# Kernel tuning notes

Hardware: AMD Instinct MI355X
Metric: run time of the kernel (lower is better)

The kernel has to match this reference:

```python
import jax, jax.numpy as jnp
import numpy as np
from jax import lax

B, N, D, H, K = 4096, 25, 256, 8, 3  # batch*frames, nodes, d_model, heads, conv kernel


def _layernorm(x, g, b, eps=1e-5):
    mu = jnp.mean(x, axis=-1, keepdims=True)
    var = jnp.var(x, axis=-1, keepdims=True)
    return (x - mu) * lax.rsqrt(var + eps) * g + b


def _conv1d(x_bdn, w):
    # x_bdn: [B, D, N], w: [D_out, D_in, K], padding=K//2 (same as torch Conv1d)
    return lax.conv_general_dilated(x_bdn, w, window_strides=(1,),
                                    padding=[(K // 2, K // 2)],
                                    dimension_numbers=('NCH', 'OIH', 'NCH'))


def setup_inputs() -> dict:
    key = jax.random.key(0)
    ks = jax.random.split(key, 12)
    x = jax.random.normal(ks[0], (B, N, D), dtype=jnp.float32)
    # symmetric adjacency with self-loops (skeleton graph surrogate)
    a = jax.random.bernoulli(ks[1], 0.3, (N, N))
    adj = a | a.T | jnp.eye(N, dtype=bool)
    cs = 1.0 / np.sqrt(D * K)
    wq = jax.random.normal(ks[2], (D, D, K), dtype=jnp.float32) * cs
    wk = jax.random.normal(ks[3], (D, D, K), dtype=jnp.float32) * cs
    wv = jax.random.normal(ks[4], (D, D, K), dtype=jnp.float32) * cs
    gq = jnp.ones((D,), jnp.float32); bq = jnp.zeros((D,), jnp.float32)
    gk = jnp.ones((D,), jnp.float32); bk = jnp.zeros((D,), jnp.float32)
    gv = jnp.ones((D,), jnp.float32); bv = jnp.zeros((D,), jnp.float32)
    rel_table = jax.random.normal(ks[5], (2 * N - 1, H), dtype=jnp.float32) * 0.02
    local_bias = jnp.zeros((H, N, N), jnp.float32)
    wo = jax.random.normal(ks[6], (D, D), dtype=jnp.float32) * (1.0 / np.sqrt(D))
    bo = jnp.zeros((D,), jnp.float32)
    return dict(x=x, adj=adj, wq=wq, wk=wk, wv=wv, gq=gq, bq=bq, gk=gk, bk=bk,
                gv=gv, bv=bv, rel_table=rel_table, local_bias=local_bias, wo=wo, bo=bo)


def reference(x, adj, wq, wk, wv, gq, bq, gk, bk, gv, bv, rel_table, local_bias, wo, bo):
    b, n, d = x.shape
    h = local_bias.shape[0]
    dk = d // h
    xp = x.transpose(0, 2, 1)  # [B, D, N]
    # conv QKV projection over node axis + per-projection LayerNorm + residual
    q = x + _layernorm(_conv1d(xp, wq).transpose(0, 2, 1), gq, bq)
    k = x + _layernorm(_conv1d(xp, wk).transpose(0, 2, 1), gk, bk)
    v = x + _layernorm(_conv1d(xp, wv).transpose(0, 2, 1), gv, bv)
    qh = q.reshape(b, n, h, dk).transpose(0, 2, 1, 3)  # [B, H, N, dk]
    kh = k.reshape(b, n, h, dk).transpose(0, 2, 1, 3)
    vh = v.reshape(b, n, h, dk).transpose(0, 2, 1, 3)
    scores = jnp.einsum('bhnd,bhmd->bhnm', qh, kh) / np.sqrt(dk)
    # relative positional bias over node indices
    coords = jnp.arange(n)
    idx = coords[:, None] - coords[None, :] + n - 1  # [N, N]
    rel = rel_table[idx].transpose(2, 0, 1)  # [H, N, N]
    scores = scores + rel[None] + local_bias[None]
    # adjacency mask (local attention): non-neighbors -> -inf
    scores = jnp.where(adj[None, None], scores, jnp.finfo(scores.dtype).min)
    attn = jax.nn.softmax(scores, axis=-1)
    out = jnp.einsum('bhnm,bhmd->bhnd', attn, vh)  # [B, H, N, dk]
    out = out.transpose(0, 2, 1, 3).reshape(b, n, d)
    return out @ wo.T + bo
```

## Files before the change

### kernel.cpp

```cpp
#include <hip/hip_runtime.h>

#define BB 4096
#define NN 25
#define DD 256
#define HH 8
#define DKH 32
#define MM (BB*NN)

typedef __bf16 bf16;
typedef bf16 bf16x8 __attribute__((ext_vector_type(8)));
typedef bf16 bf16x4 __attribute__((ext_vector_type(4)));
typedef float f32x4 __attribute__((ext_vector_type(4)));
typedef _Float16 h16;
typedef h16 h16x2 __attribute__((ext_vector_type(2)));
typedef h16 h16x4 __attribute__((ext_vector_type(4)));
typedef h16 h16x8 __attribute__((ext_vector_type(8)));

__device__ __forceinline__ void async_load16(const void* g, void* l) {
  __builtin_amdgcn_global_load_lds(
      (const __attribute__((address_space(1))) unsigned int*)g,
      (__attribute__((address_space(3))) unsigned int*)l, 16, 0, 0);
}

__global__ __launch_bounds__(256) void k_prep_xpad(const float* __restrict__ x,
                                                   bf16* __restrict__ xpad) {
  int idx = (blockIdx.x * 256 + threadIdx.x) * 8;
  const int total = BB * 27 * 256;
  if (idx >= total) return;
  int b = idx / (27 * 256);
  int rem = idx - b * 27 * 256;
  int j = rem >> 8;
  int d = rem & 255;
  bf16x8 o;
  if (j >= 1 && j <= 25) {
    const float* src = x + ((b * 25 + (j - 1)) * 256 + d);
    #pragma unroll
    for (int t = 0; t < 8; ++t) o[t] = (bf16)src[t];
  } else {
    #pragma unroll
    for (int t = 0; t < 8; ++t) o[t] = (bf16)0.0f;
  }
  *(bf16x8*)(xpad + idx) = o;
}

__global__ __launch_bounds__(256) void k_prep_misc(
    const float* __restrict__ wq, const float* __restrict__ wk, const float* __restrict__ wv,
    const float* __restrict__ rel, const float* __restrict__ lb, const float* __restrict__ wo,
    const void* __restrict__ adj_raw,
    bf16* __restrict__ Wt, bf16* __restrict__ woB, float* __restrict__ mb) {
  const int NWT = 768 * 768;
  const int NWO = 256 * 256;
  const int NMB = HH * NN * 32;
  const int total = NWT + NWO + NMB;
  for (int i = blockIdx.x * blockDim.x + threadIdx.x; i < total; i += gridDim.x * blockDim.x) {
    if (i < NWT) {
      int j = i / 768, kk = i - j * 768;
      int proj = j >> 8, jo = j & 255;
      int tap = kk >> 8, di = kk & 255;
      const float* w = (proj == 0) ? wq : ((proj == 1) ? wk : wv);
      Wt[i] = (bf16)w[(jo * 256 + di) * 3 + tap];
    } else if (i < NWT + NWO) {
      int t = i - NWT;
      woB[t] = (bf16)wo[t];
    } else {
      int t = i - NWT - NWO;
      int pair = t >> 5;
      int m = t & 31;
      int h = pair / 25, ii = pair - h * 25;
      float v = -1e30f;
      if (m < 25) {
        const unsigned char* bytes = (const unsigned char*)adj_raw;
        bool u8 = false;
        for (int s = 0; s < 625; ++s) {
          if ((s & 3) && bytes[s]) { u8 = true; break; }
        }
        int amask = u8 ? (bytes[ii * 25 + m] ? 1 : 0)
                       : (((const int*)adj_raw)[ii * 25 + m] ? 1 : 0);
        if (amask)
          v = rel[(ii - m + 24) * HH + h] + lb[h * 625 + ii * 25 + m];
      }
      mb[t] = v;
    }
  }
}

__global__ __launch_bounds__(256) void k_qkv_gemm(const bf16* __restrict__ xpad,
                                                  const bf16* __restrict__ Wt,
                                                  bf16* __restrict__ conv) {
  __shared__ bf16 As[128 * 32];
  __shared__ bf16 Bs[128 * 32];
  const int L = blockIdx.x;
  const int X = L & 7;
  const int t = L >> 3;
  const int n0 = (t % 6) * 128;
  const int m0 = (X + 8 * (t / 6)) * 128;
  const int tid = threadIdx.x;
  const int wave = tid >> 6, lane = tid & 63;
  const int quad = lane >> 4, t16 = lane & 15;
  const int wr = wave >> 1, wc = wave & 1;

  f32x4 acc[4][4];
  #pragma unroll
  for (int i = 0; i < 4; ++i)
    #pragma unroll
    for (int j = 0; j < 4; ++j) acc[i][j] = (f32x4){0.f, 0.f, 0.f, 0.f};

  const bf16* baseA[2];
  const bf16* baseB[2];
  #pragma unroll
  for (int r = 0; r < 2; ++r) {
    int c = r * 256 + wave * 64 + lane;
    int row = c >> 2, sub = c & 3;
    int gm = m0 + row;
    int b = gm / 25;
    int n = gm - b * 25;
    baseA[r] = xpad + (b * 27 + n) * 256 + sub * 8;
    baseB[r] = Wt + (n0 + row) * 768 + sub * 8;
  }

  for (int ks = 0; ks < 768; ks += 32) {
    const int tap = ks >> 8;
    const int d0 = ks & 255;
    #pragma unroll
    for (int r = 0; r < 2; ++r)
      async_load16(baseA[r] + tap * 256 + d0, As + (r * 256 + wave * 64) * 8);
    #pragma unroll
    for (int r = 0; r < 2; ++r)
      async_load16(baseB[r] + ks, Bs + (r * 256 + wave * 64) * 8);
    asm volatile("s_waitcnt vmcnt(0)" ::: "memory");
    __syncthreads();

    bf16x8 af[4], bfr[4];
    #pragma unroll
    for (int i = 0; i < 4; ++i)
      af[i] = *(const bf16x8*)(As + (wr * 64 + i * 16 + t16) * 32 + quad * 8);
    #pragma unroll
    for (int j = 0; j < 4; ++j)
      bfr[j] = *(const bf16x8*)(Bs + (wc * 64 + j * 16 + t16) * 32 + quad * 8);
    #pragma unroll
    for (int i = 0; i < 4; ++i)
      #pragma unroll
      for (int j = 0; j < 4; ++j)
        acc[i][j] = __builtin_amdgcn_mfma_f32_16x16x32_bf16(af[i], bfr[j], acc[i][j], 0, 0, 0);
    __syncthreads();
  }

  #pragma unroll
  for (int i = 0; i < 4; ++i)
    #pragma unroll
    for (int j = 0; j < 4; ++j) {
      int col = n0 + wc * 64 + j * 16 + t16;
      #pragma unroll
      for (int r = 0; r < 4; ++r) {
        int rowm = m0 + wr * 64 + i * 16 + quad * 4 + r;
        conv[rowm * 768 + col] = (bf16)acc[i][j][r];
      }
    }
}

__global__ __launch_bounds__(256, 4) void k_attn3(
    const bf16* __restrict__ conv, const float* __restrict__ x,
    const float* __restrict__ gq, const float* __restrict__ bq,
    const float* __restrict__ gk, const float* __restrict__ bk,
    const float* __restrict__ gv, const float* __restrict__ bv,
    const float* __restrict__ mb, bf16* __restrict__ attnout) {
  __shared__ bf16 Cs[19456];
  const int b = blockIdx.x;
  const int tid = threadIdx.x;
  const int wave = tid >> 6, lane = tid & 63;

  const char* slab = (const char*)(conv + (size_t)b * 19200);
  for (int c = wave; c < 38; c += 4)
    async_load16(slab + c * 1024 + lane * 16, (char*)Cs + c * 1024);
  asm volatile("s_waitcnt vmcnt(0)" ::: "memory");
  __syncthreads();

  for (int rowi = wave; rowi < 75; rowi += 4) {
    int n = rowi / 3;
    int p = rowi - n * 3;
    const int off = n * 768 + p * 256 + lane * 4;
    bf16x4 cv = *(const bf16x4*)(Cs + off);
    float v0 = (float)cv[0], v1 = (float)cv[1], v2 = (float)cv[2], v3 = (float)cv[3];
    float s = v0 + v1 + v2 + v3;
    float ss = v0 * v0 + v1 * v1 + v2 * v2 + v3 * v3;
    #pragma unroll
    for (int o = 32; o; o >>= 1) {
      s += __shfl_xor(s, o);
      ss += __shfl_xor(ss, o);
    }
    float mu = s * (1.0f / 256.0f);
    float var = ss * (1.0f / 256.0f) - mu * mu;
    float rs = rsqrtf(var + 1e-5f);
    const float* gsel = (p == 0) ? gq : ((p == 1) ? gk : gv);
    const float* bsel = (p == 0) ? bq : ((p == 1) ? bk : bv);
    const int dbase = lane * 4;
    f32x4 gg = *(const f32x4*)(gsel + dbase);
    f32x4 b2 = *(const f32x4*)(bsel + dbase);
    f32x4 xv = *(const f32x4*)(x + ((size_t)(b * 25 + n)) * 256 + dbase);
    h16x4 o;
    o[0] = (h16)((v0 - mu) * rs * gg[0] + b2[0] + xv[0]);
    o[1] = (h16)((v1 - mu) * rs * gg[1] + b2[1] + xv[1]);
    o[2] = (h16)((v2 - mu) * rs * gg[2] + b2[2] + xv[2]);
    o[3] = (h16)((v3 - mu) * rs * gg[3] + b2[3] + xv[3]);
    *(h16x4*)((h16*)Cs + off) = o;
  }
  __syncthreads();

  const h16* Ch = (const h16*)Cs;
  if (tid < HH * NN) {
    const int h = tid / 25;
    const int i = tid - h * 25;

    h16x2 qv[16];
    const h16x2* qp = (const h16x2*)(Ch + i * 768 + h * 32);
    #pragma unroll
    for (int c = 0; c < 16; ++c) qv[c] = qp[c];

    float mrow[28];
    const float* mbp = mb + (h * 25 + i) * 32;
    #pragma unroll
    for (int c = 0; c < 7; ++c) *(f32x4*)(mrow + c * 4) = *(const f32x4*)(mbp + c * 4);

    const float scale = 0.17677669529663687f;
    float sc[25];
    #pragma unroll
    for (int m = 0; m < 25; ++m) {
      const h16x2* kr = (const h16x2*)(Ch + m * 768 + 256 + h * 32);
      float d = 0.f;
      #pragma unroll
      for (int c = 0; c < 16; ++c)
        d = __builtin_amdgcn_fdot2(qv[c], kr[c], d, false);
      sc[m] = d * scale + mrow[m];
    }

    float mx = sc[0];
    #pragma unroll
    for (int m = 1; m < 25; ++m) mx = fmaxf(mx, sc[m]);
    float sum = 0.f;
    #pragma unroll
    for (int m = 0; m < 25; ++m) { sc[m] = __expf(sc[m] - mx); sum += sc[m]; }
    const float inv = 1.0f / sum;

    h16x2 acc[16];
    #pragma unroll
    for (int j = 0; j < 16; ++j) acc[j] = (h16x2){(h16)0.f, (h16)0.f};
    #pragma unroll
    for (int m = 0; m < 25; ++m) {
      h16 w = (h16)(sc[m] * inv);
      h16x2 wp = {w, w};
      const h16x2* vr = (const h16x2*)(Ch + m * 768 + 512 + h * 32);
      #pragma unroll
      for (int j = 0; j < 16; ++j)
        acc[j] = wp * vr[j] + acc[j];
    }

    bf16* dst = attnout + ((size_t)b * 25 + i) * 256 + h * 32;
    #pragma unroll
    for (int c = 0; c < 4; ++c) {
      bf16x8 o;
      #pragma unroll
      for (int j = 0; j < 4; ++j) {
        o[2 * j]     = (bf16)(float)acc[c * 4 + j][0];
        o[2 * j + 1] = (bf16)(float)acc[c * 4 + j][1];
      }
      *(bf16x8*)(dst + c * 8) = o;
    }
  }
}

__global__ __launch_bounds__(256) void k_outproj(const bf16* __restrict__ attn,
                                                 const bf16* __restrict__ woB,
                                                 const float* __restrict__ bo,
                                                 float* __restrict__ out) {
  __shared__ bf16 As[128 * 32];
  __shared__ bf16 Bs[128 * 32];
  const int L = blockIdx.x;
  const int X = L & 7;
  const int t = L >> 3;
  const int n0 = (t & 1) * 128;
  const int m0 = (X + 8 * (t >> 1)) * 128;
  const int tid = threadIdx.x;
  const int wave = tid >> 6, lane = tid & 63;
  const int quad = lane >> 4, t16 = lane & 15;
  const int wr = wave >> 1, wc = wave & 1;

  f32x4 acc[4][4];
  #pragma unroll
  for (int i = 0; i < 4; ++i)
    #pragma unroll
    for (int j = 0; j < 4; ++j) acc[i][j] = (f32x4){0.f, 0.f, 0.f, 0.f};

  const bf16* baseA[2];
  const bf16* baseB[2];
  #pragma unroll
  for (int r = 0; r < 2; ++r) {
    int c = r * 256 + wave * 64 + lane;
    int row = c >> 2, sub = c & 3;
    baseA[r] = attn + (m0 + row) * 256 + sub * 8;
    baseB[r] = woB + (n0 + row) * 256 + sub * 8;
  }

  for (int ks = 0; ks < 256; ks += 32) {
    #pragma unroll
    for (int r = 0; r < 2; ++r)
      async_load16(baseA[r] + ks, As + (r * 256 + wave * 64) * 8);
    #pragma unroll
    for (int r = 0; r < 2; ++r)
      async_load16(baseB[r] + ks, Bs + (r * 256 + wave * 64) * 8);
    asm volatile("s_waitcnt vmcnt(0)" ::: "memory");
    __syncthreads();

    bf16x8 af[4], bfr[4];
    #pragma unroll
    for (int i = 0; i < 4; ++i)
      af[i] = *(const bf16x8*)(As + (wr * 64 + i * 16 + t16) * 32 + quad * 8);
    #pragma unroll
    for (int j = 0; j < 4; ++j)
      bfr[j] = *(const bf16x8*)(Bs + (wc * 64 + j * 16 + t16) * 32 + quad * 8);
    #pragma unroll
    for (int i = 0; i < 4; ++i)
      #pragma unroll
      for (int j = 0; j < 4; ++j)
        acc[i][j] = __builtin_amdgcn_mfma_f32_16x16x32_bf16(af[i], bfr[j], acc[i][j], 0, 0, 0);
    __syncthreads();
  }

  #pragma unroll
  for (int j = 0; j < 4; ++j) {
    int col = n0 + wc * 64 + j * 16 + t16;
    float bb = bo[col];
    #pragma unroll
    for (int i = 0; i < 4; ++i)
      #pragma unroll
      for (int r = 0; r < 4; ++r) {
        int rowm = m0 + wr * 64 + i * 16 + quad * 4 + r;
        out[rowm * 256 + col] = acc[i][j][r] + bb;
      }
  }
}

extern "C" void kernel_launch(void* const* d_in, const int* in_sizes, int n_in,
                              void* d_out, int out_size, void* d_ws, size_t ws_size,
                              hipStream_t stream) {
  (void)in_sizes; (void)n_in; (void)out_size; (void)ws_size;
  const float* x  = (const float*)d_in[0];
  const void*  adj = d_in[1];
  const float* wq = (const float*)d_in[2];
  const float* wk = (const float*)d_in[3];
  const float* wv = (const float*)d_in[4];
  const float* gq = (const float*)d_in[5];
  const float* bq = (const float*)d_in[6];
  const float* gk = (const float*)d_in[7];
  const float* bk = (const float*)d_in[8];
  const float* gv = (const float*)d_in[9];
  const float* bv = (const float*)d_in[10];
  const float* rel = (const float*)d_in[11];
  const float* lb = (const float*)d_in[12];
  const float* wo = (const float*)d_in[13];
  const float* bo = (const float*)d_in[14];
  float* out = (float*)d_out;

  char* ws = (char*)d_ws;
  size_t off = 0;
  auto alloc = [&](size_t bytes) -> void* {
    void* p = ws + off;
    off += (bytes + 255) & ~(size_t)255;
    return p;
  };
  bf16* xpad = (bf16*)alloc((size_t)BB * 27 * 256 * 2);
  bf16* conv = (bf16*)alloc((size_t)MM * 768 * 2);
  bf16* attn = (bf16*)alloc((size_t)MM * 256 * 2);
  bf16* Wt   = (bf16*)alloc((size_t)768 * 768 * 2);
  bf16* woB  = (bf16*)alloc((size_t)256 * 256 * 2);
  float* mb  = (float*)alloc((size_t)HH * NN * 32 * 4);

  hipLaunchKernelGGL(k_prep_xpad, dim3(13824), dim3(256), 0, stream, x, xpad);
  hipLaunchKernelGGL(k_prep_misc, dim3(512), dim3(256), 0, stream,
                     wq, wk, wv, rel, lb, wo, adj, Wt, woB, mb);
  hipLaunchKernelGGL(k_qkv_gemm, dim3(4800), dim3(256), 0, stream, xpad, Wt, conv);
  hipLaunchKernelGGL(k_attn3, dim3(4096), dim3(256), 0, stream,
                     conv, x, gq, bq, gk, bk, gv, bv, mb, attn);
  hipLaunchKernelGGL(k_outproj, dim3(1600), dim3(256), 0, stream, attn, woB, bo, out);
}
```

Measured before the change: 556.5 us.

## Rewrite QKV conv GEMM as 256x256 double-buffered 8-wave pipelined kernel

Replaces the 128x128, 4-wave, single-buffered QKV GEMM with a 256x256 tile, 8-wave, 64-wide K-step kernel. It double-buffers LDS with async global-to-LDS loads, uses XOR-swizzled LDS layouts, and interleaves MFMA phases with the next loads under scheduling barriers and s_setprio. Block indices are remapped so consecutive blocks share tiles. The aim is to hide global load latency behind compute and raise data reuse per block. The cost is 128KB of LDS per block, heavier register use, and many barriers per K-step.

Result: no change. 549.4 us (-1.3%).

```diff
diff --git a/kernel.cpp b/kernel.cpp
--- a/kernel.cpp
+++ b/kernel.cpp
@@ -21,6 +21,10 @@
       (const __attribute__((address_space(1))) unsigned int*)g,
       (__attribute__((address_space(3))) unsigned int*)l, 16, 0, 0);
 }
+
+#define SCHED_FENCE() __builtin_amdgcn_sched_barrier(0)
+#define BARRIER() do { SCHED_FENCE(); __builtin_amdgcn_s_barrier(); SCHED_FENCE(); } while (0)
+#define WAIT_LGKM0() do { asm volatile("s_waitcnt lgkmcnt(0)" ::: "memory"); SCHED_FENCE(); } while (0)
 
 __global__ __launch_bounds__(256) void k_prep_xpad(const float* __restrict__ x,
                                                    bf16* __restrict__ xpad) {
@@ -84,76 +88,176 @@
   }
 }
 
-__global__ __launch_bounds__(256) void k_qkv_gemm(const bf16* __restrict__ xpad,
-                                                  const bf16* __restrict__ Wt,
-                                                  bf16* __restrict__ conv) {
-  __shared__ bf16 As[128 * 32];
-  __shared__ bf16 Bs[128 * 32];
+__global__ __launch_bounds__(512, 2) void k_qkv_gemm8(const bf16* __restrict__ xpad,
+                                                      const bf16* __restrict__ Wt,
+                                                      bf16* __restrict__ conv) {
+  __shared__ bf16 Ab[2][256 * 64];
+  __shared__ bf16 Bb[2][256 * 64];
+
   const int L = blockIdx.x;
-  const int X = L & 7;
-  const int t = L >> 3;
-  const int n0 = (t % 6) * 128;
-  const int m0 = (X + 8 * (t / 6)) * 128;
+  const int sw = (L & 7) * 150 + (L >> 3);
+  const int n0 = (sw % 3) * 256;
+  const int m0 = (sw / 3) * 256;
+
   const int tid = threadIdx.x;
-  const int wave = tid >> 6, lane = tid & 63;
-  const int quad = lane >> 4, t16 = lane & 15;
-  const int wr = wave >> 1, wc = wave & 1;
-
-  f32x4 acc[4][4];
-  #pragma unroll
-  for (int i = 0; i < 4; ++i)
-    #pragma unroll
-    for (int j = 0; j < 4; ++j) acc[i][j] = (f32x4){0.f, 0.f, 0.f, 0.f};
-
-  const bf16* baseA[2];
-  const bf16* baseB[2];
-  #pragma unroll
-  for (int r = 0; r < 2; ++r) {
-    int c = r * 256 + wave * 64 + lane;
-    int row = c >> 2, sub = c & 3;
+  const int lane = tid & 63, wave = tid >> 6;
+  const int t16 = lane & 15, quad = lane >> 4;
+  const int wr = wave >> 2, wc = wave & 3;
+
+  const int srow = tid >> 3;
+  const int sc = ((tid & 7) << 4) ^ ((srow & 7) << 4);
+  int aOff[4], bOff[4];
+  #pragma unroll
+  for (int q = 0; q < 4; ++q) {
+    int row = q * 64 + srow;
     int gm = m0 + row;
     int b = gm / 25;
     int n = gm - b * 25;
-    baseA[r] = xpad + (b * 27 + n) * 256 + sub * 8;
-    baseB[r] = Wt + (n0 + row) * 768 + sub * 8;
-  }
-
-  for (int ks = 0; ks < 768; ks += 32) {
-    const int tap = ks >> 8;
-    const int d0 = ks & 255;
-    #pragma unroll
-    for (int r = 0; r < 2; ++r)
-      async_load16(baseA[r] + tap * 256 + d0, As + (r * 256 + wave * 64) * 8);
-    #pragma unroll
-    for (int r = 0; r < 2; ++r)
-      async_load16(baseB[r] + ks, Bs + (r * 256 + wave * 64) * 8);
-    asm volatile("s_waitcnt vmcnt(0)" ::: "memory");
-    __syncthreads();
-
-    bf16x8 af[4], bfr[4];
-    #pragma unroll
-    for (int i = 0; i < 4; ++i)
-      af[i] = *(const bf16x8*)(As + (wr * 64 + i * 16 + t16) * 32 + quad * 8);
-    #pragma unroll
-    for (int j = 0; j < 4; ++j)
-      bfr[j] = *(const bf16x8*)(Bs + (wc * 64 + j * 16 + t16) * 32 + quad * 8);
-    #pragma unroll
-    for (int i = 0; i < 4; ++i)
-      #pragma unroll
-      for (int j = 0; j < 4; ++j)
-        acc[i][j] = __builtin_amdgcn_mfma_f32_16x16x32_bf16(af[i], bfr[j], acc[i][j], 0, 0, 0);
-    __syncthreads();
-  }
-
-  #pragma unroll
-  for (int i = 0; i < 4; ++i)
+    aOff[q] = (b * 27 + n) * 512 + sc;
+    bOff[q] = (n0 + row) * 1536 + sc;
+  }
+
+  const int axr = (t16 & 7) << 3;
+  int aoffs[2], boffs[2];
+  #pragma unroll
+  for (int kk = 0; kk < 2; ++kk) {
+    aoffs[kk] = (wr * 128 + t16) * 64 + ((kk * 32 + quad * 8) ^ axr);
+    boffs[kk] = (wc * 64 + t16) * 64 + ((kk * 32 + quad * 8) ^ axr);
+  }
+
+  f32x4 acc[8][4];
+  #pragma unroll
+  for (int i = 0; i < 8; ++i)
+    #pragma unroll
+    for (int j = 0; j < 4; ++j) acc[i][j] = (f32x4){0.f, 0.f, 0.f, 0.f};
+
+  #pragma unroll
+  for (int tt = 0; tt < 2; ++tt) {
+    char* lb = (char*)&Bb[tt][0] + wave * 1024;
+    char* la = (char*)&Ab[tt][0] + wave * 1024;
+    #pragma unroll
+    for (int q = 0; q < 4; ++q)
+      async_load16((const char*)Wt + bOff[q] + tt * 128, lb + q * 8192);
+    #pragma unroll
+    for (int q = 0; q < 4; ++q)
+      async_load16((const char*)xpad + aOff[q] + tt * 128, la + q * 8192);
+  }
+  asm volatile("s_waitcnt vmcnt(8)" ::: "memory");
+  SCHED_FENCE();
+  BARRIER();
+
+  for (int u = 0; u < 12; ++u) {
+    const int buf = u & 1;
+    const bf16* Ac = &Ab[buf][0];
+    const bf16* Bc = &Bb[buf][0];
+    const int st = u + 2;
+
+    bf16x8 aF[8], bF[8];
+
+    #pragma unroll
+    for (int i = 0; i < 4; ++i)
+      #pragma unroll
+      for (int kk = 0; kk < 2; ++kk)
+        aF[i * 2 + kk] = *(const bf16x8*)(Ac + aoffs[kk] + i * 1024);
+    #pragma unroll
+    for (int j = 0; j < 2; ++j)
+      #pragma unroll
+      for (int kk = 0; kk < 2; ++kk)
+        bF[j * 2 + kk] = *(const bf16x8*)(Bc + boffs[kk] + j * 1024);
+    BARRIER();
+    WAIT_LGKM0();
+    __builtin_amdgcn_s_setprio(1);
+    #pragma unroll
+    for (int i = 0; i < 4; ++i)
+      #pragma unroll
+      for (int j = 0; j < 2; ++j)
+        #pragma unroll
+        for (int kk = 0; kk < 2; ++kk)
+          acc[i][j] = __builtin_amdgcn_mfma_f32_16x16x32_bf16(
+              aF[i * 2 + kk], bF[j * 2 + kk], acc[i][j], 0, 0, 0);
+    __builtin_amdgcn_s_setprio(0);
+    BARRIER();
+
+    #pragma unroll
+    for (int j = 0; j < 2; ++j)
+      #pragma unroll
+      for (int kk = 0; kk < 2; ++kk)
+        bF[4 + j * 2 + kk] = *(const bf16x8*)(Bc + boffs[kk] + (2 + j) * 1024);
+    BARRIER();
+    WAIT_LGKM0();
+    __builtin_amdgcn_s_setprio(1);
+    #pragma unroll
+    for (int i = 0; i < 4; ++i)
+      #pragma unroll
+      for (int j = 0; j < 2; ++j)
+        #pragma unroll
+        for (int kk = 0; kk < 2; ++kk)
+          acc[i][2 + j] = __builtin_amdgcn_mfma_f32_16x16x32_bf16(
+              aF[i * 2 + kk], bF[4 + j * 2 + kk], acc[i][2 + j], 0, 0, 0);
+    __builtin_amdgcn_s_setprio(0);
+    BARRIER();
+
+    #pragma unroll
+    for (int i = 0; i < 4; ++i)
+      #pragma unroll
+      for (int kk = 0; kk < 2; ++kk)
+        aF[i * 2 + kk] = *(const bf16x8*)(Ac + aoffs[kk] + (4 + i) * 1024);
+    if (st < 12) {
+      char* lb = (char*)&Bb[buf][0] + wave * 1024;
+      #pragma unroll
+      for (int q = 0; q < 4; ++q)
+        async_load16((const char*)Wt + bOff[q] + st * 128, lb + q * 8192);
+    }
+    BARRIER();
+    WAIT_LGKM0();
+    __builtin_amdgcn_s_setprio(1);
+    #pragma unroll
+    for (int i = 0; i < 4; ++i)
+      #pragma unroll
+      for (int j = 0; j < 2; ++j)
+        #pragma unroll
+        for (int kk = 0; kk < 2; ++kk)
+          acc[4 + i][j] = __builtin_amdgcn_mfma_f32_16x16x32_bf16(
+              aF[i * 2 + kk], bF[j * 2 + kk], acc[4 + i][j], 0, 0, 0);
+    __builtin_amdgcn_s_setprio(0);
+    BARRIER();
+
+    if (st < 12) {
+      char* la = (char*)&Ab[buf][0] + wave * 1024;
+      const int ka = (st >> 2) * 512 + (st & 3) * 128;
+      #pragma unroll
+      for (int q = 0; q < 4; ++q)
+        async_load16((const char*)xpad + aOff[q] + ka, la + q * 8192);
+    }
+    BARRIER();
+    __builtin_amdgcn_s_setprio(1);
+    #pragma unroll
+    for (int i = 0; i < 4; ++i)
+      #pragma unroll
+      for (int j = 0; j < 2; ++j)
+        #pragma unroll
+        for (int kk = 0; kk < 2; ++kk)
+          acc[4 + i][2 + j] = __builtin_amdgcn_mfma_f32_16x16x32_bf16(
+              aF[i * 2 + kk], bF[4 + j * 2 + kk], acc[4 + i][2 + j], 0, 0, 0);
+    __builtin_amdgcn_s_setprio(0);
+    if (u < 10) {
+      asm volatile("s_waitcnt vmcnt(8)" ::: "memory");
+    } else if (u == 10) {
+      asm volatile("s_waitcnt vmcnt(0)" ::: "memory");
+    }
+    SCHED_FENCE();
+    if (u < 11) BARRIER();
+  }
+
+  #pragma unroll
+  for (int i = 0; i < 8; ++i)
     #pragma unroll
     for (int j = 0; j < 4; ++j) {
-      int col = n0 + wc * 64 + j * 16 + t16;
+      const int col = n0 + wc * 64 + j * 16 + t16;
       #pragma unroll
       for (int r = 0; r < 4; ++r) {
-        int rowm = m0 + wr * 64 + i * 16 + quad * 4 + r;
-        conv[rowm * 768 + col] = (bf16)acc[i][j][r];
+        const int rowm = m0 + wr * 128 + i * 16 + quad * 4 + r;
+        conv[(size_t)rowm * 768 + col] = (bf16)acc[i][j][r];
       }
     }
 }
@@ -377,7 +481,7 @@
   hipLaunchKernelGGL(k_prep_xpad, dim3(13824), dim3(256), 0, stream, x, xpad);
   hipLaunchKernelGGL(k_prep_misc, dim3(512), dim3(256), 0, stream,
                      wq, wk, wv, rel, lb, wo, adj, Wt, woB, mb);
-  hipLaunchKernelGGL(k_qkv_gemm, dim3(4800), dim3(256), 0, stream, xpad, Wt, conv);
+  hipLaunchKernelGGL(k_qkv_gemm8, dim3(1200), dim3(512), 0, stream, xpad, Wt, conv);
   hipLaunchKernelGGL(k_attn3, dim3(4096), dim3(256), 0, stream,
                      conv, x, gq, bq, gk, bk, gv, bv, mb, attn);
   hipLaunchKernelGGL(k_outproj, dim3(1600), dim3(256), 0, stream, attn, woB, bo, out);
```
